# Optimization experiments

Measured on AMD Instinct MI355X. Metric: run time of the kernel, lower is better.

The kernel has to match this reference:

```python
import jax, jax.numpy as jnp
import numpy as np

B, S, D = 128, 1024, 256
K = 512  # num_clusters


def setup_inputs() -> dict:
    key = jax.random.key(0)
    k1, = jax.random.split(key, 1)
    inputs = jax.random.normal(k1, (B, S, D), dtype=jnp.float32)
    # init centroids as the first K data points so no cluster is empty
    centroids = inputs.reshape(-1, D)[:K]
    return {"inputs": inputs, "centroids": centroids}


def reference(inputs, centroids):
    d = inputs.shape[-1]
    k = centroids.shape[0]
    x = inputs.reshape(-1, d)                      # [N, D]
    # squared euclidean distances via GEMM decomposition (avoids N x K x D tensor)
    x2 = jnp.sum(x * x, axis=1, keepdims=True)     # [N, 1]
    c2 = jnp.sum(centroids * centroids, axis=1)    # [K]
    dist = x2 - 2.0 * (x @ centroids.T) + c2       # [N, K]
    idx = jnp.argmin(dist, axis=-1)                # [N]
    clusters = jax.nn.one_hot(idx, k, dtype=x.dtype)   # [N, K]
    counts = jnp.sum(clusters, axis=0)             # [K]
    sums = jnp.einsum('nk,nd->kd', clusters, x)    # [K, D] scatter-reduce as GEMM
    new_centroids = sums / counts[:, None]         # [K, D]
    updated_centroids = 0.9 * centroids + 0.1 * new_centroids  # EMA update
    clusters_out = clusters.reshape(inputs.shape[:-1] + (k,))  # [B, S, K]
    return clusters_out, updated_centroids
```

## Files before the change

kernel.cpp:

```cpp
#include <hip/hip_runtime.h>
#include <hip/hip_fp16.h>

#define NPTS 131072
#define DIM  256
#define KTOT 512
#define GAP_T 0.012f

typedef unsigned short u16;
typedef _Float16 half8 __attribute__((ext_vector_type(8)));
typedef float floatx4 __attribute__((ext_vector_type(4)));

#define WS_MAIN_NEED 8394816u

__global__ __launch_bounds__(64)
void c2_kernel(const float* __restrict__ c, double* __restrict__ c2) {
  int k = blockIdx.x;
  int lane = threadIdx.x;
  const float* row = c + (size_t)k * DIM;
  double s = 0.0;
#pragma unroll
  for (int r = 0; r < DIM / 64; ++r) {
    float v = row[r * 64 + lane];
    s += (double)v * (double)v;
  }
#pragma unroll
  for (int off = 32; off > 0; off >>= 1) s += __shfl_down(s, off);
  if (lane == 0) c2[k] = s;
}

__global__ __launch_bounds__(256)
void csplit_kernel(const float* __restrict__ c, u16* __restrict__ Ch, u16* __restrict__ Cl) {
  int id = blockIdx.x * 256 + threadIdx.x;
  int n = id >> 5;
  int cg = id & 31;
  int kc = cg >> 3, cc = cg & 7;
  const float* src = c + (size_t)n * DIM + cg * 8;
  half8 hv, lv;
#pragma unroll
  for (int e = 0; e < 8; ++e) {
    float f = src[e];
    _Float16 h = (_Float16)f;
    hv[e] = h;
    lv[e] = (_Float16)(f - (float)h);
  }
  size_t dst = (size_t)n * DIM + kc * 64 + (size_t)(cc ^ (n & 7)) * 8;
  *(half8*)(Ch + dst) = hv;
  *(half8*)(Cl + dst) = lv;
}

__device__ __forceinline__ void load_lds16(const void* g, void* l) {
  __builtin_amdgcn_global_load_lds((const __attribute__((address_space(1))) void*)g,
                                   (__attribute__((address_space(3))) void*)l, 16, 0, 0);
}

__global__ __launch_bounds__(256)
void gemm_topk_kernel(const float* __restrict__ x, const u16* __restrict__ Ch,
                      const u16* __restrict__ Cl, const double* __restrict__ c2,
                      float* __restrict__ pv1, int* __restrict__ pk1, float* __restrict__ pv2) {
  __shared__ __align__(16) unsigned char smem[128 * 132 * 4];
  __shared__ float rb_v[128], rb_v2[128];
  __shared__ int rb_k[128];
  u16* Ah = (u16*)smem;
  u16* Al = Ah + 8192;
  u16* Bh = Al + 8192;
  u16* Bl = Bh + 8192;

  const int tid = threadIdx.x;
  const int bx = blockIdx.x;
  const int nblk = (bx >> 3) & 3;
  const int mblk = (bx & 7) + ((bx >> 5) << 3);
  const int m0 = mblk * 128, n0 = nblk * 128;
  const int w = tid >> 6, lane = tid & 63;
  const int wm = (w & 1) * 64, wn = (w >> 1) * 64;
  const int lm = lane & 15, quad = lane >> 4;

  floatx4 acc[4][4] = {};

  for (int kc = 0; kc < 4; ++kc) {
    const int k0 = kc * 64;
    __syncthreads();
#pragma unroll
    for (int i = 0; i < 4; ++i) {
      int s = i * 256 + tid;
      int row = s >> 3, pos = s & 7;
      size_t go = (size_t)(n0 + row) * DIM + k0 + pos * 8;
      load_lds16(Ch + go, Bh + (size_t)s * 8);
      load_lds16(Cl + go, Bl + (size_t)s * 8);
    }
#pragma unroll
    for (int i = 0; i < 4; ++i) {
      int s = i * 256 + tid;
      int row = s >> 3, kg = s & 7;
      const float4* gx = (const float4*)(x + (size_t)(m0 + row) * DIM + k0 + kg * 8);
      float4 f0 = gx[0], f1 = gx[1];
      float fv[8] = {f0.x, f0.y, f0.z, f0.w, f1.x, f1.y, f1.z, f1.w};
      half8 hv, lv;
#pragma unroll
      for (int e = 0; e < 8; ++e) {
        _Float16 h = (_Float16)fv[e];
        hv[e] = h;
        lv[e] = (_Float16)(fv[e] - (float)h);
      }
      int pos = kg ^ (row & 7);
      *(half8*)(Ah + (size_t)row * 64 + pos * 8) = hv;
      *(half8*)(Al + (size_t)row * 64 + pos * 8) = lv;
    }
    __syncthreads();

#pragma unroll
    for (int s = 0; s < 2; ++s) {
      half8 ah[4], al[4], bh[4], bl[4];
#pragma unroll
      for (int t = 0; t < 4; ++t) {
        int m = wm + t * 16 + lm;
        int pa = ((s * 4 + quad) ^ (m & 7)) * 8;
        ah[t] = *(const half8*)(Ah + (size_t)m * 64 + pa);
        al[t] = *(const half8*)(Al + (size_t)m * 64 + pa);
        int n = wn + t * 16 + lm;
        int pb = ((s * 4 + quad) ^ (n & 7)) * 8;
        bh[t] = *(const half8*)(Bh + (size_t)n * 64 + pb);
        bl[t] = *(const half8*)(Bl + (size_t)n * 64 + pb);
      }
#pragma unroll
      for (int mt = 0; mt < 4; ++mt)
#pragma unroll
        for (int nt = 0; nt < 4; ++nt) {
          acc[mt][nt] = __builtin_amdgcn_mfma_f32_16x16x32_f16(ah[mt], bh[nt], acc[mt][nt], 0, 0, 0);
          acc[mt][nt] = __builtin_amdgcn_mfma_f32_16x16x32_f16(ah[mt], bl[nt], acc[mt][nt], 0, 0, 0);
          acc[mt][nt] = __builtin_amdgcn_mfma_f32_16x16x32_f16(al[mt], bh[nt], acc[mt][nt], 0, 0, 0);
        }
    }
  }

  __syncthreads();
  float* sc = (float*)smem;
  float c2f[4];
#pragma unroll
  for (int nt = 0; nt < 4; ++nt) c2f[nt] = (float)c2[n0 + wn + nt * 16 + lm];
#pragma unroll
  for (int mt = 0; mt < 4; ++mt)
#pragma unroll
    for (int nt = 0; nt < 4; ++nt)
#pragma unroll
      for (int r = 0; r < 4; ++r) {
        int m = wm + mt * 16 + quad * 4 + r;
        int n = wn + nt * 16 + lm;
        sc[m * 132 + n] = c2f[nt] - 2.0f * acc[mt][nt][r];
      }
  __syncthreads();

  {
    int r = tid >> 1, h = tid & 1;
    const float4* rowp4 = (const float4*)(sc + r * 132 + h * 64);
    float bv = 1e30f, sv = 1e30f;
    int bk = 0;
#pragma unroll
    for (int j4 = 0; j4 < 16; ++j4) {
      float4 v4 = rowp4[j4];
      float va[4] = {v4.x, v4.y, v4.z, v4.w};
#pragma unroll
      for (int e = 0; e < 4; ++e) {
        float v = va[e];
        if (v < bv) { sv = bv; bv = v; bk = n0 + h * 64 + j4 * 4 + e; }
        else if (v < sv) sv = v;
      }
    }
    if (h == 1) { rb_v[r] = bv; rb_k[r] = bk; rb_v2[r] = sv; }
    __syncthreads();
    if (h == 0) {
      float ov = rb_v[r], ov2 = rb_v2[r];
      int ok = rb_k[r];
      float fbv, fsv; int fbk;
      if (ov < bv) { fbv = ov; fbk = ok; fsv = fminf(bv, ov2); }
      else         { fbv = bv; fbk = bk; fsv = fminf(sv, ov); }
      int m = m0 + r;
      pv1[(size_t)nblk * NPTS + m] = fbv;
      pk1[(size_t)nblk * NPTS + m] = fbk;
      pv2[(size_t)nblk * NPTS + m] = fsv;
    }
  }
}

__global__ __launch_bounds__(256)
void combine_kernel(const float* __restrict__ pv1, const int* __restrict__ pk1,
                    const float* __restrict__ pv2, int* __restrict__ idx,
                    int* __restrict__ flagcnt, int* __restrict__ flaglist) {
  int m = blockIdx.x * 256 + threadIdx.x;
  float bv = 1e30f, sv = 1e30f;
  int bk = 0;
#pragma unroll
  for (int b = 0; b < 4; ++b) {
    float v1 = pv1[(size_t)b * NPTS + m];
    int k1 = pk1[(size_t)b * NPTS + m];
    float v2 = pv2[(size_t)b * NPTS + m];
    if (v1 < bv) { sv = fminf(bv, v2); bv = v1; bk = k1; }
    else { sv = fminf(sv, v1); }
  }
  idx[m] = bk;
  if (sv - bv < GAP_T) {
    int p = atomicAdd(flagcnt, 1);
    flaglist[p] = m;
  }
}

__global__ __launch_bounds__(256)
void refine_kernel(const float* __restrict__ x, const float* __restrict__ c,
                   const double* __restrict__ c2, const int* __restrict__ flagcnt,
                   const int* __restrict__ flaglist, int* __restrict__ idx) {
  __shared__ __align__(16) float xs[DIM];
  __shared__ double rv[256];
  __shared__ int rk[256];
  int cnt = *(volatile const int*)flagcnt;
  for (int i = blockIdx.x; i < cnt; i += gridDim.x) {
    __syncthreads();
    int m = flaglist[i];
    if (threadIdx.x < 64)
      ((float4*)xs)[threadIdx.x] = ((const float4*)(x + (size_t)m * DIM))[threadIdx.x];
    __syncthreads();
    double bestv = 1e300; int bestk = 0;
#pragma unroll
    for (int half = 0; half < 2; ++half) {
      int k = half * 256 + threadIdx.x;
      const float* crow = c + (size_t)k * DIM;
      double dacc = 0.0;
#pragma unroll
      for (int dc = 0; dc < 8; ++dc) {
        float f = 0.0f;
#pragma unroll
        for (int d = 0; d < 32; ++d) f = fmaf(xs[dc * 32 + d], crow[dc * 32 + d], f);
        dacc += (double)f;
      }
      double s = c2[k] - 2.0 * dacc;
      if (s < bestv || (s == bestv && k < bestk)) { bestv = s; bestk = k; }
    }
    rv[threadIdx.x] = bestv; rk[threadIdx.x] = bestk;
    __syncthreads();
    for (int off = 128; off > 0; off >>= 1) {
      if (threadIdx.x < off) {
        double v = rv[threadIdx.x + off]; int kk = rk[threadIdx.x + off];
        if (v < rv[threadIdx.x] || (v == rv[threadIdx.x] && kk < rk[threadIdx.x])) {
          rv[threadIdx.x] = v; rk[threadIdx.x] = kk;
        }
      }
      __syncthreads();
    }
    if (threadIdx.x == 0) idx[m] = rk[0];
  }
}

__global__ __launch_bounds__(256)
void onehot_kernel(const int* __restrict__ idx, float* __restrict__ out) {
  __shared__ int bk[32];
  int b = blockIdx.x;
  if (threadIdx.x < 32) bk[threadIdx.x] = idx[b * 32 + threadIdx.x];
  __syncthreads();
  float4* o = (float4*)(out + (size_t)b * 32 * KTOT);
#pragma unroll
  for (int j = 0; j < 16; ++j) {
    int f4 = j * 256 + threadIdx.x;
    int p = f4 >> 7;
    int n4 = (f4 & 127) * 4;
    int k = bk[p];
    float4 v;
    v.x = (k == n4 + 0) ? 1.0f : 0.0f;
    v.y = (k == n4 + 1) ? 1.0f : 0.0f;
    v.z = (k == n4 + 2) ? 1.0f : 0.0f;
    v.w = (k == n4 + 3) ? 1.0f : 0.0f;
    o[f4] = v;
  }
}

__global__ __launch_bounds__(256)
void hist_kernel(const int* __restrict__ idx, int* __restrict__ counts) {
  __shared__ int h[KTOT];
  int t = threadIdx.x;
#pragma unroll
  for (int i = 0; i < KTOT / 256; ++i) h[i * 256 + t] = 0;
  __syncthreads();
  int base = blockIdx.x * 1024 + t;
#pragma unroll
  for (int j = 0; j < 4; ++j) atomicAdd(&h[idx[base + j * 256]], 1);
  __syncthreads();
#pragma unroll
  for (int i = 0; i < KTOT / 256; ++i) {
    int v = h[i * 256 + t];
    if (v) atomicAdd(&counts[i * 256 + t], v);
  }
}

__global__ __launch_bounds__(512)
void scan_kernel(const int* __restrict__ counts, int* __restrict__ offsets,
                 int* __restrict__ cursors) {
  __shared__ int s[KTOT];
  int t = threadIdx.x;
  int mine = counts[t];
  s[t] = mine;
  __syncthreads();
  for (int off = 1; off < KTOT; off <<= 1) {
    int v = (t >= off) ? s[t - off] : 0;
    __syncthreads();
    s[t] += v;
    __syncthreads();
  }
  int excl = s[t] - mine;
  offsets[t] = excl;
  cursors[t] = excl;
  if (t == KTOT - 1) offsets[KTOT] = s[t];
}

__global__ __launch_bounds__(256)
void scatter_kernel(const int* __restrict__ idx, int* __restrict__ cursors,
                    int* __restrict__ plist) {
  int base = blockIdx.x * 1024 + threadIdx.x;
#pragma unroll
  for (int j = 0; j < 4; ++j) {
    int n = base + j * 256;
    int k = idx[n];
    int pos = atomicAdd(&cursors[k], 1);
    plist[pos] = n;
  }
}

__global__ __launch_bounds__(256)
void gathersum_flat_kernel(const float* __restrict__ x, const int* __restrict__ plist,
                           const int* __restrict__ offsets, float* __restrict__ sums) {
  __shared__ int offs[KTOT + 1];
  for (int t = threadIdx.x; t < KTOT + 1; t += 256) offs[t] = offsets[t];
  __syncthreads();
  const int w = threadIdx.x >> 6, lane = threadIdx.x & 63;
  const int wid = blockIdx.x * 4 + w;
  const int p0 = wid * 32, p1 = p0 + 32;

  int lo = 0, hi = KTOT;
  while (hi - lo > 1) { int mid = (lo + hi) >> 1; if (offs[mid] <= p0) lo = mid; else hi = mid; }
  int k = lo;

  float4 acc = make_float4(0.f, 0.f, 0.f, 0.f);
  bool any = false;
#pragma unroll 4
  for (int i = p0; i < p1; ++i) {
    while (i >= offs[k + 1]) {
      if (any) {
        float* dst = sums + (size_t)k * DIM + lane * 4;
        atomicAdd(dst + 0, acc.x); atomicAdd(dst + 1, acc.y);
        atomicAdd(dst + 2, acc.z); atomicAdd(dst + 3, acc.w);
        acc = make_float4(0.f, 0.f, 0.f, 0.f);
        any = false;
      }
      ++k;
    }
    int pid = plist[i];
    float4 v = ((const float4*)x)[(size_t)pid * 64 + lane];
    acc.x += v.x; acc.y += v.y; acc.z += v.z; acc.w += v.w;
    any = true;
  }
  if (any) {
    float* dst = sums + (size_t)k * DIM + lane * 4;
    atomicAdd(dst + 0, acc.x); atomicAdd(dst + 1, acc.y);
    atomicAdd(dst + 2, acc.z); atomicAdd(dst + 3, acc.w);
  }
}

__global__ __launch_bounds__(256)
void ema_kernel(const float* __restrict__ c, const float* __restrict__ sums,
                const int* __restrict__ counts, float* __restrict__ outc) {
  int k = blockIdx.x;
  int d = threadIdx.x;
  float cnt = (float)counts[k];
  size_t o = (size_t)k * DIM + d;
  float nc = sums[o] / cnt;
  outc[o] = 0.9f * c[o] + 0.1f * nc;
}

#define GB 4
#define SLICES 8
__global__ __launch_bounds__(256)
void sums_kernel(const float* __restrict__ x, const int* __restrict__ idx,
                 float* __restrict__ sums, int* __restrict__ counts) {
  const int groups = KTOT / GB;
  const int group = blockIdx.x % groups;
  const int slice = blockIdx.x / groups;
  const int kg0 = group * GB;
  const int tid = threadIdx.x;
  const int lane = tid & 63;
  const int w = tid >> 6;
  const int per_slice = NPTS / SLICES;
  const int nbeg = slice * per_slice;

  float4 acc[GB];
  int cnt[GB];
#pragma unroll
  for (int j = 0; j < GB; ++j) { acc[j] = make_float4(0.f, 0.f, 0.f, 0.f); cnt[j] = 0; }

  for (int it = 0; it < per_slice; it += 256) {
    int n = nbeg + it + tid;
    int k = idx[n];
#pragma unroll
    for (int j = 0; j < GB; ++j) {
      unsigned long long m = __ballot(k == kg0 + j);
      while (m) {
        int src = __ffsll((unsigned long long)m) - 1;
        int nn = __shfl(n, src);
        float4 v = ((const float4*)(x + (size_t)nn * DIM))[lane];
        acc[j].x += v.x; acc[j].y += v.y; acc[j].z += v.z; acc[j].w += v.w;
        cnt[j]++;
        m &= (m - 1);
      }
    }
  }

  __shared__ __align__(16) float lacc[4][GB][DIM];
  __shared__ int lcnt[4][GB];
#pragma unroll
  for (int j = 0; j < GB; ++j) ((float4*)&lacc[w][j][0])[lane] = acc[j];
  if (lane == 0) {
#pragma unroll
    for (int j = 0; j < GB; ++j) lcnt[w][j] = cnt[j];
  }
  __syncthreads();
#pragma unroll
  for (int j = 0; j < GB; ++j) {
    float s = lacc[0][j][tid] + lacc[1][j][tid] + lacc[2][j][tid] + lacc[3][j][tid];
    atomicAdd(&sums[(size_t)(kg0 + j) * DIM + tid], s);
  }
  if (tid < GB) {
    int ct = lcnt[0][tid] + lcnt[1][tid] + lcnt[2][tid] + lcnt[3][tid];
    atomicAdd(&counts[kg0 + tid], ct);
  }
}

#define MP 64
#define KT 64
#define DT 32
__global__ __launch_bounds__(256, 2)
void assign_kernel_r1(const float* __restrict__ x, const float* __restrict__ c,
                      const double* __restrict__ c2, float* __restrict__ out,
                      int* __restrict__ idx_out) {
  __shared__ __align__(16) float xs[DIM * MP];
  __shared__ __align__(16) float cs[DT * KT];
  const int tid = threadIdx.x;
  const int p0 = blockIdx.x * MP;
  const int tp = tid & 15;
  const int tk = tid >> 4;
  {
    const int p = tid >> 2;
    const int dg = tid & 3;
    const float4* x4 = (const float4*)(x + (size_t)(p0 + p) * DIM);
#pragma unroll
    for (int r = 0; r < 16; ++r) {
      int d4 = r * 4 + dg;
      float4 v = x4[d4];
      int dbase = d4 * 4;
      xs[(dbase + 0) * MP + p] = v.x;
      xs[(dbase + 1) * MP + p] = v.y;
      xs[(dbase + 2) * MP + p] = v.z;
      xs[(dbase + 3) * MP + p] = v.w;
    }
  }
  double best[4]; int bestk[4];
#pragma unroll
  for (int i = 0; i < 4; ++i) { best[i] = 1e300; bestk[i] = 0; }
  for (int kc = 0; kc < KTOT / KT; ++kc) {
    const int k0 = kc * KT;
    double dacc[4][4];
#pragma unroll
    for (int i = 0; i < 4; ++i)
#pragma unroll
      for (int j = 0; j < 4; ++j) dacc[i][j] = 0.0;
    for (int dc = 0; dc < DIM / DT; ++dc) {
      __syncthreads();
      {
        const int kl = tid >> 2;
        const int dg = tid & 3;
        const float4* c4 = (const float4*)(c + (size_t)(k0 + kl) * DIM + dc * DT);
#pragma unroll
        for (int h = 0; h < 2; ++h) {
          int dq = h * 4 + dg;
          float4 v = c4[dq];
          int dbase = dq * 4;
          cs[(dbase + 0) * KT + kl] = v.x;
          cs[(dbase + 1) * KT + kl] = v.y;
          cs[(dbase + 2) * KT + kl] = v.z;
          cs[(dbase + 3) * KT + kl] = v.w;
        }
      }
      __syncthreads();
      float acc[4][4];
#pragma unroll
      for (int i = 0; i < 4; ++i)
#pragma unroll
        for (int j = 0; j < 4; ++j) acc[i][j] = 0.0f;
#pragma unroll
      for (int d = 0; d < DT; ++d) {
        float4 xv = ((const float4*)(xs + (size_t)(dc * DT + d) * MP))[tp];
        float4 cv = ((const float4*)(cs + (size_t)d * KT))[tk];
        float xa[4] = {xv.x, xv.y, xv.z, xv.w};
        float ca[4] = {cv.x, cv.y, cv.z, cv.w};
#pragma unroll
        for (int i = 0; i < 4; ++i)
#pragma unroll
          for (int j = 0; j < 4; ++j) acc[i][j] = fmaf(xa[i], ca[j], acc[i][j]);
      }
#pragma unroll
      for (int i = 0; i < 4; ++i)
#pragma unroll
        for (int j = 0; j < 4; ++j) dacc[i][j] += (double)acc[i][j];
    }
#pragma unroll
    for (int j = 0; j < 4; ++j) {
      int k = k0 + tk * 4 + j;
      double c2v = c2[k];
#pragma unroll
      for (int i = 0; i < 4; ++i) {
        double s = c2v - 2.0 * dacc[i][j];
        if (s < best[i]) { best[i] = s; bestk[i] = k; }
      }
    }
  }
  __syncthreads();
  double* redv = (double*)cs;
  int* redk = (int*)xs;
  int* bk = (int*)xs + 1024;
#pragma unroll
  for (int i = 0; i < 4; ++i) {
    int p = tp * 4 + i;
    redv[tk * MP + p] = best[i];
    redk[tk * MP + p] = bestk[i];
  }
  __syncthreads();
  if (tid < MP) {
    int p = tid;
    double bv = redv[p]; int bkk = redk[p];
#pragma unroll
    for (int t = 1; t < 16; ++t) {
      double v = redv[t * MP + p]; int kk = redk[t * MP + p];
      if (v < bv || (v == bv && kk < bkk)) { bv = v; bkk = kk; }
    }
    bk[p] = bkk;
    idx_out[p0 + p] = bkk;
  }
  __syncthreads();
  float* orow = out + (size_t)p0 * KTOT;
  for (int l = tid; l < MP * KTOT; l += 256) {
    int p = l >> 9;
    int k = l & (KTOT - 1);
    orow[l] = (k == bk[p]) ? 1.0f : 0.0f;
  }
}

extern "C" void kernel_launch(void* const* d_in, const int* in_sizes, int n_in,
                              void* d_out, int out_size, void* d_ws, size_t ws_size,
                              hipStream_t stream) {
  const float* x = (const float*)d_in[0];
  const float* c = (const float*)d_in[1];
  float* out = (float*)d_out;
  float* outc = out + (size_t)NPTS * KTOT;

  char* ws = (char*)d_ws;

  if (ws_size >= WS_MAIN_NEED) {
    double* c2   = (double*)(ws + 0);
    u16* Ch      = (u16*)(ws + 4096);
    u16* Cl      = (u16*)(ws + 266240);
    int* idx     = (int*)(ws + 528384);
    float* pv1   = (float*)(ws + 1052672);
    int* pk1     = (int*)(ws + 3149824);
    float* pv2   = (float*)(ws + 5246976);
    float* sums  = (float*)(ws + 7344128);
    int* counts  = (int*)(ws + 7868416);
    int* flagcnt = (int*)(ws + 7870464);
    int* flaglist= (int*)(ws + 7870528);
    int* offsets = (int*)(ws + 1052672);
    int* cursors = (int*)(ws + 1052672 + 4096);
    int* plist   = (int*)(ws + 5246976);

    hipMemsetAsync(sums, 0, (size_t)(KTOT * DIM + KTOT) * 4, stream);
    hipMemsetAsync(flagcnt, 0, 64, stream);
    c2_kernel<<<KTOT, 64, 0, stream>>>(c, c2);
    csplit_kernel<<<64, 256, 0, stream>>>(c, Ch, Cl);
    gemm_topk_kernel<<<4096, 256, 0, stream>>>(x, Ch, Cl, c2, pv1, pk1, pv2);
    combine_kernel<<<NPTS / 256, 256, 0, stream>>>(pv1, pk1, pv2, idx, flagcnt, flaglist);
    refine_kernel<<<1024, 256, 0, stream>>>(x, c, c2, flagcnt, flaglist, idx);
    onehot_kernel<<<NPTS / 32, 256, 0, stream>>>(idx, out);
    hist_kernel<<<NPTS / 1024, 256, 0, stream>>>(idx, counts);
    scan_kernel<<<1, 512, 0, stream>>>(counts, offsets, cursors);
    scatter_kernel<<<NPTS / 1024, 256, 0, stream>>>(idx, cursors, plist);
    gathersum_flat_kernel<<<NPTS / 32 / 4, 256, 0, stream>>>(x, plist, offsets, sums);
    ema_kernel<<<KTOT, DIM, 0, stream>>>(c, sums, counts, outc);
  } else {
    double* c2  = (double*)ws;
    int* idx    = (int*)(ws + 4096);
    float* sums = (float*)(ws + 4096 + 524288);
    int* counts = (int*)(ws + 4096 + 524288 + 524288);
    hipMemsetAsync(sums, 0, (size_t)(KTOT * DIM + KTOT) * 4, stream);
    c2_kernel<<<KTOT, 64, 0, stream>>>(c, c2);
    assign_kernel_r1<<<NPTS / MP, 256, 0, stream>>>(x, c, c2, out, idx);
    sums_kernel<<<(KTOT / GB) * SLICES, 256, 0, stream>>>(x, idx, sums, counts);
    ema_kernel<<<KTOT, DIM, 0, stream>>>(c, sums, counts, outc);
  }
}
```

Before: 696.4 us.

## Use single fp16 GEMM pass with wider refine gap and register top-2 reduction

Drops the split-fp16 (hi/lo) error-compensated GEMM and uses plain fp16 MFMA, cutting the MFMA count and LDS traffic to a third. To keep argmin exact, it widens the gap threshold so many more points are flagged for the exact refine pass. The top-2 selection now runs in registers with cross-lane shuffles instead of staging scores through LDS. The one-hot output uses nontemporal stores. The risk is a much larger refine workload if many points fall within the wider gap.

```diff
diff --git a/kernel.cpp b/kernel.cpp
--- a/kernel.cpp
+++ b/kernel.cpp
@@ -4,7 +4,7 @@
 #define NPTS 131072
 #define DIM  256
 #define KTOT 512
-#define GAP_T 0.012f
+#define GAP_T 0.5f
 
 typedef unsigned short u16;
 typedef _Float16 half8 __attribute__((ext_vector_type(8)));
@@ -29,23 +29,17 @@
 }
 
 __global__ __launch_bounds__(256)
-void csplit_kernel(const float* __restrict__ c, u16* __restrict__ Ch, u16* __restrict__ Cl) {
+void csplit_kernel(const float* __restrict__ c, u16* __restrict__ Ch) {
   int id = blockIdx.x * 256 + threadIdx.x;
   int n = id >> 5;
   int cg = id & 31;
   int kc = cg >> 3, cc = cg & 7;
   const float* src = c + (size_t)n * DIM + cg * 8;
-  half8 hv, lv;
-#pragma unroll
-  for (int e = 0; e < 8; ++e) {
-    float f = src[e];
-    _Float16 h = (_Float16)f;
-    hv[e] = h;
-    lv[e] = (_Float16)(f - (float)h);
-  }
+  half8 hv;
+#pragma unroll
+  for (int e = 0; e < 8; ++e) hv[e] = (_Float16)src[e];
   size_t dst = (size_t)n * DIM + kc * 64 + (size_t)(cc ^ (n & 7)) * 8;
   *(half8*)(Ch + dst) = hv;
-  *(half8*)(Cl + dst) = lv;
 }
 
 __device__ __forceinline__ void load_lds16(const void* g, void* l) {
@@ -55,15 +49,12 @@
 
 __global__ __launch_bounds__(256)
 void gemm_topk_kernel(const float* __restrict__ x, const u16* __restrict__ Ch,
-                      const u16* __restrict__ Cl, const double* __restrict__ c2,
+                      const double* __restrict__ c2,
                       float* __restrict__ pv1, int* __restrict__ pk1, float* __restrict__ pv2) {
-  __shared__ __align__(16) unsigned char smem[128 * 132 * 4];
-  __shared__ float rb_v[128], rb_v2[128];
-  __shared__ int rb_k[128];
-  u16* Ah = (u16*)smem;
-  u16* Al = Ah + 8192;
-  u16* Bh = Al + 8192;
-  u16* Bl = Bh + 8192;
+  __shared__ __align__(16) u16 Ah[128 * 64];
+  __shared__ __align__(16) u16 Bh[128 * 64];
+  __shared__ float mv1[128][2], mv2[128][2];
+  __shared__ int mk1[128][2];
 
   const int tid = threadIdx.x;
   const int bx = blockIdx.x;
@@ -85,7 +76,6 @@
       int row = s >> 3, pos = s & 7;
       size_t go = (size_t)(n0 + row) * DIM + k0 + pos * 8;
       load_lds16(Ch + go, Bh + (size_t)s * 8);
-      load_lds16(Cl + go, Bl + (size_t)s * 8);
     }
 #pragma unroll
     for (int i = 0; i < 4; ++i) {
@@ -94,90 +84,78 @@
       const float4* gx = (const float4*)(x + (size_t)(m0 + row) * DIM + k0 + kg * 8);
       float4 f0 = gx[0], f1 = gx[1];
       float fv[8] = {f0.x, f0.y, f0.z, f0.w, f1.x, f1.y, f1.z, f1.w};
-      half8 hv, lv;
-#pragma unroll
-      for (int e = 0; e < 8; ++e) {
-        _Float16 h = (_Float16)fv[e];
-        hv[e] = h;
-        lv[e] = (_Float16)(fv[e] - (float)h);
-      }
+      half8 hv;
+#pragma unroll
+      for (int e = 0; e < 8; ++e) hv[e] = (_Float16)fv[e];
       int pos = kg ^ (row & 7);
       *(half8*)(Ah + (size_t)row * 64 + pos * 8) = hv;
-      *(half8*)(Al + (size_t)row * 64 + pos * 8) = lv;
     }
     __syncthreads();
 
 #pragma unroll
     for (int s = 0; s < 2; ++s) {
-      half8 ah[4], al[4], bh[4], bl[4];
+      half8 ah[4], bh[4];
 #pragma unroll
       for (int t = 0; t < 4; ++t) {
         int m = wm + t * 16 + lm;
         int pa = ((s * 4 + quad) ^ (m & 7)) * 8;
         ah[t] = *(const half8*)(Ah + (size_t)m * 64 + pa);
-        al[t] = *(const half8*)(Al + (size_t)m * 64 + pa);
         int n = wn + t * 16 + lm;
         int pb = ((s * 4 + quad) ^ (n & 7)) * 8;
         bh[t] = *(const half8*)(Bh + (size_t)n * 64 + pb);
-        bl[t] = *(const half8*)(Bl + (size_t)n * 64 + pb);
       }
 #pragma unroll
       for (int mt = 0; mt < 4; ++mt)
 #pragma unroll
-        for (int nt = 0; nt < 4; ++nt) {
+        for (int nt = 0; nt < 4; ++nt)
           acc[mt][nt] = __builtin_amdgcn_mfma_f32_16x16x32_f16(ah[mt], bh[nt], acc[mt][nt], 0, 0, 0);
-          acc[mt][nt] = __builtin_amdgcn_mfma_f32_16x16x32_f16(ah[mt], bl[nt], acc[mt][nt], 0, 0, 0);
-          acc[mt][nt] = __builtin_amdgcn_mfma_f32_16x16x32_f16(al[mt], bh[nt], acc[mt][nt], 0, 0, 0);
-        }
-    }
-  }
-
-  __syncthreads();
-  float* sc = (float*)smem;
+    }
+  }
+
   float c2f[4];
 #pragma unroll
   for (int nt = 0; nt < 4; ++nt) c2f[nt] = (float)c2[n0 + wn + nt * 16 + lm];
+
 #pragma unroll
   for (int mt = 0; mt < 4; ++mt)
 #pragma unroll
-    for (int nt = 0; nt < 4; ++nt)
-#pragma unroll
-      for (int r = 0; r < 4; ++r) {
-        int m = wm + mt * 16 + quad * 4 + r;
-        int n = wn + nt * 16 + lm;
-        sc[m * 132 + n] = c2f[nt] - 2.0f * acc[mt][nt][r];
-      }
-  __syncthreads();
-
-  {
-    int r = tid >> 1, h = tid & 1;
-    const float4* rowp4 = (const float4*)(sc + r * 132 + h * 64);
-    float bv = 1e30f, sv = 1e30f;
-    int bk = 0;
-#pragma unroll
-    for (int j4 = 0; j4 < 16; ++j4) {
-      float4 v4 = rowp4[j4];
-      float va[4] = {v4.x, v4.y, v4.z, v4.w};
-#pragma unroll
-      for (int e = 0; e < 4; ++e) {
-        float v = va[e];
-        if (v < bv) { sv = bv; bv = v; bk = n0 + h * 64 + j4 * 4 + e; }
+    for (int r = 0; r < 4; ++r) {
+      float bv = 1e30f, sv = 1e30f;
+      int bk = 0;
+#pragma unroll
+      for (int nt = 0; nt < 4; ++nt) {
+        float v = c2f[nt] - 2.0f * acc[mt][nt][r];
+        int n = n0 + wn + nt * 16 + lm;
+        if (v < bv) { sv = bv; bv = v; bk = n; }
         else if (v < sv) sv = v;
       }
-    }
-    if (h == 1) { rb_v[r] = bv; rb_k[r] = bk; rb_v2[r] = sv; }
-    __syncthreads();
-    if (h == 0) {
-      float ov = rb_v[r], ov2 = rb_v2[r];
-      int ok = rb_k[r];
-      float fbv, fsv; int fbk;
-      if (ov < bv) { fbv = ov; fbk = ok; fsv = fminf(bv, ov2); }
-      else         { fbv = bv; fbk = bk; fsv = fminf(sv, ov); }
-      int m = m0 + r;
-      pv1[(size_t)nblk * NPTS + m] = fbv;
-      pk1[(size_t)nblk * NPTS + m] = fbk;
-      pv2[(size_t)nblk * NPTS + m] = fsv;
-    }
+#pragma unroll
+      for (int off = 1; off < 16; off <<= 1) {
+        float ov = __shfl_xor(bv, off);
+        int ok = __shfl_xor(bk, off);
+        float osv = __shfl_xor(sv, off);
+        if (ov < bv || (ov == bv && ok < bk)) { sv = fminf(bv, osv); bv = ov; bk = ok; }
+        else sv = fminf(sv, ov);
+      }
+      if (lm == 0) {
+        int mr = wm + mt * 16 + quad * 4 + r;
+        int sl = w >> 1;
+        mv1[mr][sl] = bv; mk1[mr][sl] = bk; mv2[mr][sl] = sv;
+      }
+    }
+  __syncthreads();
+  if (tid < 128) {
+    float bv = mv1[tid][0], sv = mv2[tid][0];
+    int bk = mk1[tid][0];
+    float ov = mv1[tid][1], osv = mv2[tid][1];
+    int ok = mk1[tid][1];
+    if (ov < bv) { sv = fminf(bv, osv); bv = ov; bk = ok; }
+    else sv = fminf(sv, ov);
+    int m = m0 + tid;
+    pv1[(size_t)nblk * NPTS + m] = bv;
+    pk1[(size_t)nblk * NPTS + m] = bk;
+    pv2[(size_t)nblk * NPTS + m] = sv;
+    (void)ok;
   }
 }
 
@@ -254,19 +232,19 @@
   int b = blockIdx.x;
   if (threadIdx.x < 32) bk[threadIdx.x] = idx[b * 32 + threadIdx.x];
   __syncthreads();
-  float4* o = (float4*)(out + (size_t)b * 32 * KTOT);
+  floatx4* o = (floatx4*)(out + (size_t)b * 32 * KTOT);
 #pragma unroll
   for (int j = 0; j < 16; ++j) {
     int f4 = j * 256 + threadIdx.x;
     int p = f4 >> 7;
     int n4 = (f4 & 127) * 4;
     int k = bk[p];
-    float4 v;
-    v.x = (k == n4 + 0) ? 1.0f : 0.0f;
-    v.y = (k == n4 + 1) ? 1.0f : 0.0f;
-    v.z = (k == n4 + 2) ? 1.0f : 0.0f;
-    v.w = (k == n4 + 3) ? 1.0f : 0.0f;
-    o[f4] = v;
+    floatx4 v;
+    v[0] = (k == n4 + 0) ? 1.0f : 0.0f;
+    v[1] = (k == n4 + 1) ? 1.0f : 0.0f;
+    v[2] = (k == n4 + 2) ? 1.0f : 0.0f;
+    v[3] = (k == n4 + 3) ? 1.0f : 0.0f;
+    __builtin_nontemporal_store(v, &o[f4]);
   }
 }
 
@@ -561,7 +539,6 @@
   if (ws_size >= WS_MAIN_NEED) {
     double* c2   = (double*)(ws + 0);
     u16* Ch      = (u16*)(ws + 4096);
-    u16* Cl      = (u16*)(ws + 266240);
     int* idx     = (int*)(ws + 528384);
     float* pv1   = (float*)(ws + 1052672);
     int* pk1     = (int*)(ws + 3149824);
@@ -577,8 +554,8 @@
     hipMemsetAsync(sums, 0, (size_t)(KTOT * DIM + KTOT) * 4, stream);
     hipMemsetAsync(flagcnt, 0, 64, stream);
     c2_kernel<<<KTOT, 64, 0, stream>>>(c, c2);
-    csplit_kernel<<<64, 256, 0, stream>>>(c, Ch, Cl);
-    gemm_topk_kernel<<<4096, 256, 0, stream>>>(x, Ch, Cl, c2, pv1, pk1, pv2);
+    csplit_kernel<<<64, 256, 0, stream>>>(c, Ch);
+    gemm_topk_kernel<<<4096, 256, 0, stream>>>(x, Ch, c2, pv1, pk1, pv2);
     combine_kernel<<<NPTS / 256, 256, 0, stream>>>(pv1, pk1, pv2, idx, flagcnt, flaglist);
     refine_kernel<<<1024, 256, 0, stream>>>(x, c, c2, flagcnt, flaglist, idx);
     onehot_kernel<<<NPTS / 32, 256, 0, stream>>>(idx, out);
```

Result: slower. 876.0 us (+25.8%).
